# Optimization experiments

Measured on AMD Instinct MI355X. Metric: run time of the kernel, lower is better.

Reference implementation:

```python
import jax, jax.numpy as jnp
import numpy as np

B, S, D, E, TOPK = 8, 4096, 1024, 64, 2
TEMP = 0.01


def setup_inputs() -> dict:
    key = jax.random.key(0)
    k_x, k_w1, k_b1, k_w2, k_b2 = jax.random.split(key, 5)
    x = jax.random.normal(k_x, (B, S, D), dtype=jnp.float32)
    # torch.nn.Linear default init ~ U(-1/sqrt(fan_in), 1/sqrt(fan_in)); scale ok for reference
    W1 = jax.random.normal(k_w1, (D, 2 * D), dtype=jnp.float32) * (1.0 / np.sqrt(D))
    b1 = jax.random.normal(k_b1, (2 * D,), dtype=jnp.float32) * 0.01
    W2 = jax.random.normal(k_w2, (2 * D, E), dtype=jnp.float32) * (1.0 / np.sqrt(2 * D))
    b2 = jax.random.normal(k_b2, (E,), dtype=jnp.float32) * 0.01
    return {"x": x, "W1": W1, "b1": b1, "W2": W2, "b2": b2}


def reference(x, W1, b1, W2, b2):
    # 2-layer MLP router: [B,S,D] -> [B,S,2D] -> [B,S,E]
    h = jax.nn.relu(jnp.einsum('bsd,df->bsf', x, W1) + b1)
    logits = jnp.einsum('bsf,fe->bse', h, W2) + b2
    # top-k over experts
    top_k_logits, indices = jax.lax.top_k(logits, TOPK)  # [B,S,K]
    # scatter top-k logits into a -inf-filled tensor: equivalent to masking,
    # since scattered values equal logits at those positions
    keep = jax.nn.one_hot(indices, E, dtype=bool).any(axis=-2)  # [B,S,E]
    sparse_logits = jnp.where(keep, logits, -jnp.inf)
    router_output = jax.nn.softmax(sparse_logits, axis=-1)
    ori_router_output = jax.nn.softmax(logits / TEMP, axis=-1)
    return (ori_router_output, router_output, indices)
```

## Files before the change

kernel.cpp:

```cpp
#include <hip/hip_runtime.h>
#include <math.h>
#include <stdint.h>

#define M_TOK 32768
#define D_IN  1024
#define F_HID 2048
#define E_EXP 64

#define O_ORI 0
#define O_RTR (M_TOK * E_EXP)
#define O_IDX (2 * M_TOK * E_EXP)

typedef _Float16 half8 __attribute__((ext_vector_type(8)));
typedef float    f32x4 __attribute__((ext_vector_type(4)));
typedef unsigned int uint32;
typedef uint32   u32x4 __attribute__((ext_vector_type(4)));

#define WS_XH  ((size_t)0)
#define WS_XL  (WS_XH  + (size_t)M_TOK * D_IN * 2)
#define WS_W1H (WS_XL  + (size_t)M_TOK * D_IN * 2)
#define WS_W1L (WS_W1H + (size_t)D_IN * F_HID * 2)
#define WS_W2H (WS_W1L + (size_t)D_IN * F_HID * 2)
#define WS_W2L (WS_W2H + (size_t)F_HID * E_EXP * 2)
#define WS_NEED (WS_W2L + (size_t)F_HID * E_EXP * 2)

__device__ __forceinline__ void split_sc(float v, float sc, unsigned short& h, unsigned short& l) {
    const _Float16 hh = (_Float16)v;
    const float hf = (float)hh;
    const _Float16 hs = (_Float16)(hf * sc);
    const _Float16 ls = (_Float16)((v - hf) * sc);
    h = __builtin_bit_cast(unsigned short, hs);
    l = __builtin_bit_cast(unsigned short, ls);
}


__global__ void split_x_k(const float* __restrict__ x,
                          unsigned short* __restrict__ xh, unsigned short* __restrict__ xl) {
    size_t i = ((size_t)blockIdx.x * 256 + threadIdx.x) * 4;
    const float4 v = *(const float4*)&x[i];
    ushort4 h, l;
    split_sc(v.x, 64.f, h.x, l.x); split_sc(v.y, 64.f, h.y, l.y);
    split_sc(v.z, 64.f, h.z, l.z); split_sc(v.w, 64.f, h.w, l.w);
    *(ushort4*)&xh[i] = h;
    *(ushort4*)&xl[i] = l;
}

__global__ void split_w1t_k(const float* __restrict__ W1,
                            unsigned short* __restrict__ wh, unsigned short* __restrict__ wl) {
    __shared__ float t[32][33];
    const int d0 = blockIdx.x * 32;
    const int f0 = blockIdx.y * 32;
    const int r  = threadIdx.x >> 3;
    const int c4 = (threadIdx.x & 7) * 4;
    const float4 v = *(const float4*)&W1[(size_t)(d0 + r) * F_HID + f0 + c4];
    t[r][c4 + 0] = v.x; t[r][c4 + 1] = v.y; t[r][c4 + 2] = v.z; t[r][c4 + 3] = v.w;
    __syncthreads();
    ushort4 h, l;
    split_sc(t[c4 + 0][r], 64.f, h.x, l.x);
    split_sc(t[c4 + 1][r], 64.f, h.y, l.y);
    split_sc(t[c4 + 2][r], 64.f, h.z, l.z);
    split_sc(t[c4 + 3][r], 64.f, h.w, l.w);
    *(ushort4*)&wh[(size_t)(f0 + r) * D_IN + d0 + c4] = h;
    *(ushort4*)&wl[(size_t)(f0 + r) * D_IN + d0 + c4] = l;
}

__global__ void split_w2f_k(const float* __restrict__ W2,
                            unsigned short* __restrict__ wh, unsigned short* __restrict__ wl) {
    const int s  = blockIdx.x;
    const int nt = threadIdx.x >> 6;
    const int l  = threadIdx.x & 63;
    const int fb = s * 32 + (l >> 4) * 8;
    const int e  = nt * 16 + (l & 15);
    unsigned short h[8], lo[8];
#pragma unroll
    for (int j = 0; j < 8; ++j)
        split_sc(W2[(size_t)(fb + j) * E_EXP + e], 16.f, h[j], lo[j]);
    const size_t base = ((size_t)(s * 4 + nt) * 64 + l) * 8;
    ((ushort4*)&wh[base])[0] = make_ushort4(h[0], h[1], h[2], h[3]);
    ((ushort4*)&wh[base])[1] = make_ushort4(h[4], h[5], h[6], h[7]);
    ((ushort4*)&wl[base])[0] = make_ushort4(lo[0], lo[1], lo[2], lo[3]);
    ((ushort4*)&wl[base])[1] = make_ushort4(lo[4], lo[5], lo[6], lo[7]);
}


__device__ __forceinline__ uint32 swz(uint32 o) { return o ^ (((o >> 7) & 7u) << 4); }

#define STAGE16(SRCP, DSTP) \
    __builtin_amdgcn_global_load_lds((const __attribute__((address_space(1))) void*)(SRCP), \
                                     (__attribute__((address_space(3))) void*)(DSTP), 16, 0, 0)


__launch_bounds__(512, 2)
__global__ void router_one(const unsigned short* __restrict__ xh, const unsigned short* __restrict__ xl,
                           const unsigned short* __restrict__ w1h, const unsigned short* __restrict__ w1l,
                           const unsigned short* __restrict__ w2fh, const unsigned short* __restrict__ w2fl,
                           const float* __restrict__ b1, const float* __restrict__ b2,
                           float* __restrict__ out)
{
    __shared__ __align__(16) unsigned char lds[131072];

    const int tid  = threadIdx.x;
    const int lane = tid & 63;
    const int w    = tid >> 6;
    const int c15  = lane & 15;
    const int g    = lane >> 4;
    const int wr   = w >> 2;
    const int wc   = w & 3;

    const size_t tok0 = (size_t)blockIdx.x * 128;

    uint32 arow, ahalf, brow[2], bhalf[2];
    {
        const uint32 sA = swz((uint32)(tid * 16));
        arow = sA >> 6; ahalf = (sA & 63u) >> 1;
#pragma unroll
        for (int j = 0; j < 2; ++j) {
            const uint32 sB = swz((uint32)(j * 8192 + w * 1024 + lane * 16));
            brow[j] = sB >> 6; bhalf[j] = (sB & 63u) >> 1;
        }
    }

    uint32 offA[4], offB[4];
#pragma unroll
    for (int m = 0; m < 4; ++m)
        offA[m] = swz((uint32)((wr * 64 + m * 16 + c15) * 64 + g * 16));
#pragma unroll
    for (int n = 0; n < 4; ++n)
        offB[n] = swz((uint32)((wc * 64 + n * 16 + c15) * 64 + g * 16));

    f32x4 acc2[4];
#pragma unroll
    for (int nt = 0; nt < 4; ++nt) acc2[nt] = (f32x4){0.f, 0.f, 0.f, 0.f};

#define STAGE_T(T, BUF, F0) do {                                                     \
    const int d0_ = (T) * 32;                                                        \
    const size_t asrc = (tok0 + arow) * D_IN + (size_t)(d0_ + (int)ahalf);           \
    STAGE16(xh + asrc, lds + (BUF) * 16384 + w * 1024);                              \
    STAGE16(xl + asrc, lds + (BUF) * 16384 + 8192 + w * 1024);                       \
    _Pragma("unroll")                                                                \
    for (int j = 0; j < 2; ++j) {                                                    \
        const size_t bsrc = ((size_t)(F0) + brow[j]) * D_IN + (size_t)(d0_ + (int)bhalf[j]); \
        STAGE16(w1h + bsrc, lds + 32768 + (BUF) * 32768 + j * 8192 + w * 1024);      \
        STAGE16(w1l + bsrc, lds + 32768 + (BUF) * 32768 + 16384 + j * 8192 + w * 1024); \
    } } while (0)

#pragma unroll 1
    for (int fc = 0; fc < F_HID; fc += 256) {
        f32x4 acc[4][4];
#pragma unroll
        for (int m = 0; m < 4; ++m)
#pragma unroll
            for (int n = 0; n < 4; ++n) acc[m][n] = (f32x4){0.f, 0.f, 0.f, 0.f};

        __syncthreads();
        STAGE_T(0, 0, fc);
        STAGE_T(1, 1, fc);

#pragma unroll 1
        for (int t = 0; t < 32; ++t) {
            if (t < 31) asm volatile("s_waitcnt vmcnt(6)" ::: "memory");
            else        asm volatile("s_waitcnt vmcnt(0)" ::: "memory");
            __builtin_amdgcn_s_barrier();
            const unsigned char* Ab = lds + (t & 1) * 16384;
            const unsigned char* Bb = lds + 32768 + (t & 1) * 32768;

            half8 b1f[4], b2f[4];
#pragma unroll
            for (int n = 0; n < 4; ++n) {
                b1f[n] = *(const half8*)(Bb + offB[n]);
                b2f[n] = *(const half8*)(Bb + 16384 + offB[n]);
            }
            half8 a1f[2], a2f[2];
#pragma unroll
            for (int m = 0; m < 2; ++m) {
                a1f[m] = *(const half8*)(Ab + offA[m]);
                a2f[m] = *(const half8*)(Ab + 8192 + offA[m]);
            }
            __builtin_amdgcn_s_setprio(1);
#pragma unroll
            for (int m = 0; m < 2; ++m)
#pragma unroll
                for (int n = 0; n < 4; ++n) {
                    acc[m][n] = __builtin_amdgcn_mfma_f32_16x16x32_f16(a1f[m], b1f[n], acc[m][n], 0, 0, 0);
                    acc[m][n] = __builtin_amdgcn_mfma_f32_16x16x32_f16(a1f[m], b2f[n], acc[m][n], 0, 0, 0);
                    acc[m][n] = __builtin_amdgcn_mfma_f32_16x16x32_f16(a2f[m], b1f[n], acc[m][n], 0, 0, 0);
                }
            __builtin_amdgcn_s_setprio(0);
#pragma unroll
            for (int m = 0; m < 2; ++m) {
                a1f[m] = *(const half8*)(Ab + offA[2 + m]);
                a2f[m] = *(const half8*)(Ab + 8192 + offA[2 + m]);
            }
            __builtin_amdgcn_s_setprio(1);
#pragma unroll
            for (int m = 0; m < 2; ++m)
#pragma unroll
                for (int n = 0; n < 4; ++n) {
                    acc[2 + m][n] = __builtin_amdgcn_mfma_f32_16x16x32_f16(a1f[m], b1f[n], acc[2 + m][n], 0, 0, 0);
                    acc[2 + m][n] = __builtin_amdgcn_mfma_f32_16x16x32_f16(a1f[m], b2f[n], acc[2 + m][n], 0, 0, 0);
                    acc[2 + m][n] = __builtin_amdgcn_mfma_f32_16x16x32_f16(a2f[m], b1f[n], acc[2 + m][n], 0, 0, 0);
                }
            __builtin_amdgcn_s_setprio(0);
            __builtin_amdgcn_s_barrier();
            if (t + 2 < 32) STAGE_T(t + 2, t & 1, fc);
        }

        {
            float bv[4];
#pragma unroll
            for (int n = 0; n < 4; ++n) bv[n] = b1[fc + wc * 64 + n * 16 + c15];
#pragma unroll
            for (int m = 0; m < 4; ++m)
#pragma unroll
                for (int n = 0; n < 4; ++n)
#pragma unroll
                    for (int r = 0; r < 4; ++r) {
                        float hv = acc[m][n][r] * (1.f / 4096.f) + bv[n];
                        hv = fmaxf(hv, 0.f);
                        const _Float16 hh = (_Float16)hv;
                        const float hf = (float)hh;
                        const _Float16 hsv = (_Float16)(hf * 16.f);
                        const _Float16 lsv = (_Float16)((hv - hf) * 16.f);
                        const uint32 pk = (uint32)__builtin_bit_cast(unsigned short, hsv)
                                        | ((uint32)__builtin_bit_cast(unsigned short, lsv) << 16);
                        const int tok = wr * 64 + m * 16 + g * 4 + r;
                        const int fl  = wc * 64 + n * 16 + c15;
                        *(uint32*)(lds + tok * 1024 + ((fl * 4) ^ ((tok & 15) << 4))) = pk;
                    }
        }
        __syncthreads();

        {
            const int tokA = w * 16 + c15;
#pragma unroll
            for (int s = 0; s < 8; ++s) {
                const int kf = s * 32 + g * 8;
                const int sg = (fc >> 5) + s;
                half8 bf1[4], bf2[4];
#pragma unroll
                for (int nt = 0; nt < 4; ++nt) {
                    const size_t base = ((size_t)(sg * 4 + nt) * 64 + lane) * 8;
                    bf1[nt] = *(const half8*)&w2fh[base];
                    bf2[nt] = *(const half8*)&w2fl[base];
                }
                const u32x4 q0 = *(const u32x4*)(lds + tokA * 1024 + (((kf    ) * 4) ^ (c15 << 4)));
                const u32x4 q1 = *(const u32x4*)(lds + tokA * 1024 + (((kf + 4) * 4) ^ (c15 << 4)));
                u32x4 hi4, lo4;
                hi4[0] = __builtin_amdgcn_perm(q0[1], q0[0], 0x05040100u);
                hi4[1] = __builtin_amdgcn_perm(q0[3], q0[2], 0x05040100u);
                hi4[2] = __builtin_amdgcn_perm(q1[1], q1[0], 0x05040100u);
                hi4[3] = __builtin_amdgcn_perm(q1[3], q1[2], 0x05040100u);
                lo4[0] = __builtin_amdgcn_perm(q0[1], q0[0], 0x07060302u);
                lo4[1] = __builtin_amdgcn_perm(q0[3], q0[2], 0x07060302u);
                lo4[2] = __builtin_amdgcn_perm(q1[1], q1[0], 0x07060302u);
                lo4[3] = __builtin_amdgcn_perm(q1[3], q1[2], 0x07060302u);
                const half8 a1 = __builtin_bit_cast(half8, hi4);
                const half8 a2 = __builtin_bit_cast(half8, lo4);
#pragma unroll
                for (int nt = 0; nt < 4; ++nt) {
                    acc2[nt] = __builtin_amdgcn_mfma_f32_16x16x32_f16(a1, bf1[nt], acc2[nt], 0, 0, 0);
                    acc2[nt] = __builtin_amdgcn_mfma_f32_16x16x32_f16(a1, bf2[nt], acc2[nt], 0, 0, 0);
                    acc2[nt] = __builtin_amdgcn_mfma_f32_16x16x32_f16(a2, bf1[nt], acc2[nt], 0, 0, 0);
                }
            }
        }
    }
#undef STAGE_T

    __syncthreads();
    float* ls = (float*)lds;
#pragma unroll
    for (int nt = 0; nt < 4; ++nt)
#pragma unroll
        for (int r = 0; r < 4; ++r) {
            const int tl = w * 16 + g * 4 + r;
            ls[tl * 68 + nt * 16 + c15] = acc2[nt][r] * (1.f / 256.f);
        }
    __syncthreads();

    const int e = lane;
    const float be = b2[e];
#pragma unroll 1
    for (int i = 0; i < 16; ++i) {
        const float l = ls[(w * 16 + i) * 68 + e] + be;

        float v = l; int idx = e;
#pragma unroll
        for (int m = 32; m >= 1; m >>= 1) {
            const float ov = __shfl_xor(v, m, 64);
            const int   oi = __shfl_xor(idx, m, 64);
            if (ov > v || (ov == v && oi < idx)) { v = ov; idx = oi; }
        }
        const float m1 = v; const int i1 = idx;

        v = (e == i1) ? -INFINITY : l; idx = e;
#pragma unroll
        for (int m = 32; m >= 1; m >>= 1) {
            const float ov = __shfl_xor(v, m, 64);
            const int   oi = __shfl_xor(idx, m, 64);
            if (ov > v || (ov == v && oi < idx)) { v = ov; idx = oi; }
        }
        const int i2 = idx;

        const float ex = expf((l - m1) * 100.0f);
        float s = ex;
#pragma unroll
        for (int m = 32; m >= 1; m >>= 1) s += __shfl_xor(s, m, 64);
        const float ori = ex / s;

        const float q = (e == i1 || e == i2) ? expf(l - m1) : 0.f;
        float s2 = q;
#pragma unroll
        for (int m = 32; m >= 1; m >>= 1) s2 += __shfl_xor(s2, m, 64);
        const float rtr = q / s2;

        const size_t tok = tok0 + (size_t)w * 16 + i;
        out[O_ORI + tok * E_EXP + e] = ori;
        out[O_RTR + tok * E_EXP + e] = rtr;
        if (e == 0) {
            out[O_IDX + tok * 2 + 0] = (float)i1;
            out[O_IDX + tok * 2 + 1] = (float)i2;
        }
    }
}


#define BT  64
#define NB  256

__launch_bounds__(256, 2)
__global__ void router_mfma(const unsigned short* __restrict__ xh, const unsigned short* __restrict__ xl,
                            const unsigned short* __restrict__ w1h, const unsigned short* __restrict__ w1l,
                            const unsigned short* __restrict__ w2fh, const unsigned short* __restrict__ w2fl,
                            const float* __restrict__ b1, const float* __restrict__ b2,
                            float* __restrict__ out)
{
    __shared__ __align__(16) unsigned char xs_h[BT * 64];
    __shared__ __align__(16) unsigned char xs_l[BT * 64];
    __shared__ __align__(16) unsigned char w1s_h[NB * 64];
    __shared__ __align__(16) unsigned char w1s_l[NB * 64];
    __shared__ __align__(16) unsigned char hsbuf[BT * 132 * 4];

    const int tid  = threadIdx.x;
    const int lane = tid & 63;
    const int w    = tid >> 6;
    const int c15  = lane & 15;
    const int g    = lane >> 4;
    const size_t tok0 = (size_t)blockIdx.x * BT;

    uint32* hs = (uint32*)hsbuf;
    float*  ls = (float*)hsbuf;

    f32x4 acc2h[4], acc2x[4];
#pragma unroll
    for (int nt = 0; nt < 4; ++nt) {
        acc2h[nt] = (f32x4){0.f, 0.f, 0.f, 0.f};
        acc2x[nt] = (f32x4){0.f, 0.f, 0.f, 0.f};
    }

    const uint32 kqb = (uint32)g * 16u;

    for (int fc = 0; fc < F_HID; fc += NB) {
        f32x4 ahh[4][4], axx[4][4];
#pragma unroll
        for (int mt = 0; mt < 4; ++mt)
#pragma unroll
            for (int nt = 0; nt < 4; ++nt) {
                ahh[mt][nt] = (f32x4){0.f, 0.f, 0.f, 0.f};
                axx[mt][nt] = (f32x4){0.f, 0.f, 0.f, 0.f};
            }

        for (int d0 = 0; d0 < D_IN; d0 += 32) {
            __syncthreads();
            {
                uint32 o = (uint32)w * 1024u + (uint32)lane * 16u;
                uint32 s = swz(o);
                uint32 r = s >> 6, hb = (s & 63u) >> 1;
                const unsigned short* sp;
                sp = xh + (tok0 + r) * D_IN + (size_t)(d0 + (int)hb);
                STAGE16(sp, xs_h + (size_t)w * 1024);
                sp = xl + (tok0 + r) * D_IN + (size_t)(d0 + (int)hb);
                STAGE16(sp, xs_l + (size_t)w * 1024);
#pragma unroll
                for (int q = 0; q < 4; ++q) {
                    const uint32 c_ = (uint32)(q * 4 + w);
                    uint32 o2 = c_ * 1024u + (uint32)lane * 16u;
                    uint32 s2 = swz(o2);
                    uint32 r2 = s2 >> 6, hb2 = (s2 & 63u) >> 1;
                    sp = w1h + ((size_t)(fc + (int)r2)) * D_IN + (size_t)(d0 + (int)hb2);
                    STAGE16(sp, w1s_h + (size_t)c_ * 1024);
                    sp = w1l + ((size_t)(fc + (int)r2)) * D_IN + (size_t)(d0 + (int)hb2);
                    STAGE16(sp, w1s_l + (size_t)c_ * 1024);
                }
            }
            __syncthreads();

            half8 ah[4], al[4], bh[4], bl[4];
#pragma unroll
            for (int mt = 0; mt < 4; ++mt) {
                const uint32 off = swz((uint32)(mt * 16 + c15) * 64u + kqb);
                ah[mt] = *(const half8*)(xs_h + off);
                al[mt] = *(const half8*)(xs_l + off);
            }
#pragma unroll
            for (int nt = 0; nt < 4; ++nt) {
                const uint32 row = (uint32)(w * 64 + nt * 16 + c15);
                const uint32 off = swz(row * 64u + kqb);
                bh[nt] = *(const half8*)(w1s_h + off);
                bl[nt] = *(const half8*)(w1s_l + off);
            }
#pragma unroll
            for (int mt = 0; mt < 4; ++mt)
#pragma unroll
                for (int nt = 0; nt < 4; ++nt) {
                    ahh[mt][nt] = __builtin_amdgcn_mfma_f32_16x16x32_f16(ah[mt], bh[nt], ahh[mt][nt], 0, 0, 0);
                    axx[mt][nt] = __builtin_amdgcn_mfma_f32_16x16x32_f16(ah[mt], bl[nt], axx[mt][nt], 0, 0, 0);
                    axx[mt][nt] = __builtin_amdgcn_mfma_f32_16x16x32_f16(al[mt], bh[nt], axx[mt][nt], 0, 0, 0);
                }
        }

        const int fl0 = (w & 1) * 64;
#pragma unroll
        for (int phase = 0; phase < 2; ++phase) {
            if ((w >> 1) == phase) {
#pragma unroll
                for (int nt = 0; nt < 4; ++nt) {
                    const float b1v = b1[fc + w * 64 + nt * 16 + c15];
#pragma unroll
                    for (int mt = 0; mt < 4; ++mt) {
#pragma unroll
                        for (int r = 0; r < 4; ++r) {
                            float hv = (ahh[mt][nt][r] + axx[mt][nt][r]) * (1.f / 4096.f) + b1v;
                            hv = fmaxf(hv, 0.f);
                            const _Float16 hhv0 = (_Float16)hv;
                            const float hf = (float)hhv0;
                            const _Float16 hhv = (_Float16)(hf * 16.f);
                            const _Float16 hlv = (_Float16)((hv - hf) * 16.f);
                            uint32 pk = (uint32)__builtin_bit_cast(unsigned short, hhv)
                                      | ((uint32)__builtin_bit_cast(unsigned short, hlv) << 16);
                            const int t = mt * 16 + g * 4 + r;
                            hs[t * 132 + fl0 + nt * 16 + c15] = pk;
                        }
                    }
                }
            }
            __syncthreads();
            const int tA = w * 16 + c15;
#pragma unroll
            for (int ktl = 0; ktl < 4; ++ktl) {
                const u32x4 q0 = *(const u32x4*)&hs[tA * 132 + ktl * 32 + g * 8];
                const u32x4 q1 = *(const u32x4*)&hs[tA * 132 + ktl * 32 + g * 8 + 4];
                u32x4 hi4, lo4;
                hi4[0] = __builtin_amdgcn_perm(q0[1], q0[0], 0x05040100u);
                hi4[1] = __builtin_amdgcn_perm(q0[3], q0[2], 0x05040100u);
                hi4[2] = __builtin_amdgcn_perm(q1[1], q1[0], 0x05040100u);
                hi4[3] = __builtin_amdgcn_perm(q1[3], q1[2], 0x05040100u);
                lo4[0] = __builtin_amdgcn_perm(q0[1], q0[0], 0x07060302u);
                lo4[1] = __builtin_amdgcn_perm(q0[3], q0[2], 0x07060302u);
                lo4[2] = __builtin_amdgcn_perm(q1[1], q1[0], 0x07060302u);
                lo4[3] = __builtin_amdgcn_perm(q1[3], q1[2], 0x07060302u);
                const half8 a_h = __builtin_bit_cast(half8, hi4);
                const half8 a_l = __builtin_bit_cast(half8, lo4);
                const int sg = (fc >> 5) + phase * 4 + ktl;
#pragma unroll
                for (int nt = 0; nt < 4; ++nt) {
                    const size_t base = ((size_t)(sg * 4 + nt) * 64 + lane) * 8;
                    const half8 b_h = *(const half8*)&w2fh[base];
                    const half8 b_l = *(const half8*)&w2fl[base];
                    acc2h[nt] = __builtin_amdgcn_mfma_f32_16x16x32_f16(a_h, b_h, acc2h[nt], 0, 0, 0);
                    acc2x[nt] = __builtin_amdgcn_mfma_f32_16x16x32_f16(a_h, b_l, acc2x[nt], 0, 0, 0);
                    acc2x[nt] = __builtin_amdgcn_mfma_f32_16x16x32_f16(a_l, b_h, acc2x[nt], 0, 0, 0);
                }
            }
            __syncthreads();
        }
    }

#pragma unroll
    for (int nt = 0; nt < 4; ++nt)
#pragma unroll
        for (int r = 0; r < 4; ++r) {
            const int t = w * 16 + g * 4 + r;
            ls[t * 68 + nt * 16 + c15] = (acc2h[nt][r] + acc2x[nt][r]) * (1.f / 256.f);
        }
    __syncthreads();

    const int e = lane;
    const float be = b2[e];
#pragma unroll 1
    for (int i = 0; i < 16; ++i) {
        const float l = ls[(w * 16 + i) * 68 + e] + be;

        float v = l; int idx = e;
#pragma unroll
        for (int m = 32; m >= 1; m >>= 1) {
            const float ov = __shfl_xor(v, m, 64);
            const int   oi = __shfl_xor(idx, m, 64);
            if (ov > v || (ov == v && oi < idx)) { v = ov; idx = oi; }
        }
        const float m1 = v; const int i1 = idx;

        v = (e == i1) ? -INFINITY : l; idx = e;
#pragma unroll
        for (int m = 32; m >= 1; m >>= 1) {
            const float ov = __shfl_xor(v, m, 64);
            const int   oi = __shfl_xor(idx, m, 64);
            if (ov > v || (ov == v && oi < idx)) { v = ov; idx = oi; }
        }
        const int i2 = idx;

        const float ex = expf((l - m1) * 100.0f);
        float s = ex;
#pragma unroll
        for (int m = 32; m >= 1; m >>= 1) s += __shfl_xor(s, m, 64);
        const float ori = ex / s;

        const float q = (e == i1 || e == i2) ? expf(l - m1) : 0.f;
        float s2 = q;
#pragma unroll
        for (int m = 32; m >= 1; m >>= 1) s2 += __shfl_xor(s2, m, 64);
        const float rtr = q / s2;

        const size_t tok = tok0 + (size_t)w * 16 + i;
        out[O_ORI + tok * E_EXP + e] = ori;
        out[O_RTR + tok * E_EXP + e] = rtr;
        if (e == 0) {
            out[O_IDX + tok * 2 + 0] = (float)i1;
            out[O_IDX + tok * 2 + 1] = (float)i2;
        }
    }
}


extern "C" void kernel_launch(void* const* d_in, const int* in_sizes, int n_in,
                              void* d_out, int out_size, void* d_ws, size_t ws_size,
                              hipStream_t stream) {
    const float* x  = (const float*)d_in[0];
    const float* W1 = (const float*)d_in[1];
    const float* b1 = (const float*)d_in[2];
    const float* W2 = (const float*)d_in[3];
    const float* b2 = (const float*)d_in[4];
    float* out = (float*)d_out;

    unsigned char* ws = (unsigned char*)d_ws;
    unsigned short* xh  = (unsigned short*)(ws + WS_XH);
    unsigned short* xl  = (unsigned short*)(ws + WS_XL);
    unsigned short* w1h = (unsigned short*)(ws + WS_W1H);
    unsigned short* w1l = (unsigned short*)(ws + WS_W1L);
    unsigned short* w2h = (unsigned short*)(ws + WS_W2H);
    unsigned short* w2l = (unsigned short*)(ws + WS_W2L);

    hipLaunchKernelGGL(split_x_k,  dim3(M_TOK * D_IN / 4 / 256), dim3(256), 0, stream, x, xh, xl);
    hipLaunchKernelGGL(split_w1t_k, dim3(D_IN / 32, F_HID / 32), dim3(256), 0, stream, W1, w1h, w1l);
    hipLaunchKernelGGL(split_w2f_k, dim3(F_HID / 32), dim3(256), 0, stream, W2, w2h, w2l);

    if (ws_size >= WS_NEED) {
        hipLaunchKernelGGL(router_one, dim3(M_TOK / 128), dim3(512), 0, stream,
                           xh, xl, w1h, w1l, w2h, w2l, b1, b2, out);
    } else {
        hipLaunchKernelGGL(router_mfma, dim3(M_TOK / BT), dim3(256), 0, stream,
                           xh, xl, w1h, w1l, w2h, w2l, b1, b2, out);
    }
}
```

Measured before the change: 504.9 us.

## Triple-buffer W1 GEMM LDS staging and interleave loads with MFMA phases

Grows the LDS ring from two to three buffers so the next-next tile can be staged into a free buffer while the current one is read. The main loop is split into four MFMA phases, one per B column tile, with the A-tile and B-tile global→LDS copies spread between them. This aims to hide global-load issue and the LDS read latency behind matrix math instead of staging after a trailing barrier. In exchange it adds many more s_barriers and lgkmcnt waits per iteration and holds all four A fragments in registers, which raises register pressure.

```diff
diff --git a/kernel.cpp b/kernel.cpp
--- a/kernel.cpp
+++ b/kernel.cpp
@@ -90,6 +90,9 @@
                                      (__attribute__((address_space(3))) void*)(DSTP), 16, 0, 0)
 
 
+#define A_BUF(b)  ((b) * 16384)
+#define B_BUF(b)  (49152 + (b) * 32768)
+
 __launch_bounds__(512, 2)
 __global__ void router_one(const unsigned short* __restrict__ xh, const unsigned short* __restrict__ xl,
                            const unsigned short* __restrict__ w1h, const unsigned short* __restrict__ w1l,
@@ -97,7 +100,7 @@
                            const float* __restrict__ b1, const float* __restrict__ b2,
                            float* __restrict__ out)
 {
-    __shared__ __align__(16) unsigned char lds[131072];
+    __shared__ __align__(16) unsigned char lds[147456];
 
     const int tid  = threadIdx.x;
     const int lane = tid & 63;
@@ -132,17 +135,18 @@
 #pragma unroll
     for (int nt = 0; nt < 4; ++nt) acc2[nt] = (f32x4){0.f, 0.f, 0.f, 0.f};
 
-#define STAGE_T(T, BUF, F0) do {                                                     \
+#define STAGE_A(T, WB, F0) do {                                                      \
     const int d0_ = (T) * 32;                                                        \
     const size_t asrc = (tok0 + arow) * D_IN + (size_t)(d0_ + (int)ahalf);           \
-    STAGE16(xh + asrc, lds + (BUF) * 16384 + w * 1024);                              \
-    STAGE16(xl + asrc, lds + (BUF) * 16384 + 8192 + w * 1024);                       \
-    _Pragma("unroll")                                                                \
-    for (int j = 0; j < 2; ++j) {                                                    \
-        const size_t bsrc = ((size_t)(F0) + brow[j]) * D_IN + (size_t)(d0_ + (int)bhalf[j]); \
-        STAGE16(w1h + bsrc, lds + 32768 + (BUF) * 32768 + j * 8192 + w * 1024);      \
-        STAGE16(w1l + bsrc, lds + 32768 + (BUF) * 32768 + 16384 + j * 8192 + w * 1024); \
-    } } while (0)
+    STAGE16(xh + asrc, lds + A_BUF(WB) + w * 1024);                                  \
+    STAGE16(xl + asrc, lds + A_BUF(WB) + 8192 + w * 1024);                           \
+} while (0)
+#define STAGE_B(T, WB, F0, J) do {                                                   \
+    const int d0_ = (T) * 32;                                                        \
+    const size_t bsrc = ((size_t)(F0) + brow[J]) * D_IN + (size_t)(d0_ + (int)bhalf[J]); \
+    STAGE16(w1h + bsrc, lds + B_BUF(WB) + (J) * 8192 + w * 1024);                    \
+    STAGE16(w1l + bsrc, lds + B_BUF(WB) + 16384 + (J) * 8192 + w * 1024);            \
+} while (0)
 
 #pragma unroll 1
     for (int fc = 0; fc < F_HID; fc += 256) {
@@ -153,58 +157,87 @@
             for (int n = 0; n < 4; ++n) acc[m][n] = (f32x4){0.f, 0.f, 0.f, 0.f};
 
         __syncthreads();
-        STAGE_T(0, 0, fc);
-        STAGE_T(1, 1, fc);
+        STAGE_A(0, 0, fc); STAGE_B(0, 0, fc, 0); STAGE_B(0, 0, fc, 1);
+        STAGE_A(1, 1, fc); STAGE_B(1, 1, fc, 0); STAGE_B(1, 1, fc, 1);
 
 #pragma unroll 1
         for (int t = 0; t < 32; ++t) {
             if (t < 31) asm volatile("s_waitcnt vmcnt(6)" ::: "memory");
             else        asm volatile("s_waitcnt vmcnt(0)" ::: "memory");
             __builtin_amdgcn_s_barrier();
-            const unsigned char* Ab = lds + (t & 1) * 16384;
-            const unsigned char* Bb = lds + 32768 + (t & 1) * 32768;
-
-            half8 b1f[4], b2f[4];
-#pragma unroll
-            for (int n = 0; n < 4; ++n) {
-                b1f[n] = *(const half8*)(Bb + offB[n]);
-                b2f[n] = *(const half8*)(Bb + 16384 + offB[n]);
-            }
-            half8 a1f[2], a2f[2];
-#pragma unroll
-            for (int m = 0; m < 2; ++m) {
+            const int rb = t % 3;
+            const int wb = (t + 2) % 3;
+            const bool do_stage = (t + 2 < 32);
+            const unsigned char* Ab = lds + A_BUF(rb);
+            const unsigned char* Bb = lds + B_BUF(rb);
+
+            half8 a1f[4], a2f[4], b1f[4], b2f[4];
+
+#pragma unroll
+            for (int m = 0; m < 4; ++m) {
                 a1f[m] = *(const half8*)(Ab + offA[m]);
                 a2f[m] = *(const half8*)(Ab + 8192 + offA[m]);
             }
+            b1f[0] = *(const half8*)(Bb + offB[0]);
+            b2f[0] = *(const half8*)(Bb + 16384 + offB[0]);
+            if (do_stage) STAGE_A(t + 2, wb, fc);
+            __builtin_amdgcn_s_barrier();
+            asm volatile("s_waitcnt lgkmcnt(0)" ::: "memory");
             __builtin_amdgcn_s_setprio(1);
 #pragma unroll
-            for (int m = 0; m < 2; ++m)
-#pragma unroll
-                for (int n = 0; n < 4; ++n) {
-                    acc[m][n] = __builtin_amdgcn_mfma_f32_16x16x32_f16(a1f[m], b1f[n], acc[m][n], 0, 0, 0);
-                    acc[m][n] = __builtin_amdgcn_mfma_f32_16x16x32_f16(a1f[m], b2f[n], acc[m][n], 0, 0, 0);
-                    acc[m][n] = __builtin_amdgcn_mfma_f32_16x16x32_f16(a2f[m], b1f[n], acc[m][n], 0, 0, 0);
-                }
+            for (int m = 0; m < 4; ++m) {
+                acc[m][0] = __builtin_amdgcn_mfma_f32_16x16x32_f16(a1f[m], b1f[0], acc[m][0], 0, 0, 0);
+                acc[m][0] = __builtin_amdgcn_mfma_f32_16x16x32_f16(a1f[m], b2f[0], acc[m][0], 0, 0, 0);
+                acc[m][0] = __builtin_amdgcn_mfma_f32_16x16x32_f16(a2f[m], b1f[0], acc[m][0], 0, 0, 0);
+            }
             __builtin_amdgcn_s_setprio(0);
-#pragma unroll
-            for (int m = 0; m < 2; ++m) {
-                a1f[m] = *(const half8*)(Ab + offA[2 + m]);
-                a2f[m] = *(const half8*)(Ab + 8192 + offA[2 + m]);
-            }
+            __builtin_amdgcn_s_barrier();
+
+            b1f[1] = *(const half8*)(Bb + offB[1]);
+            b2f[1] = *(const half8*)(Bb + 16384 + offB[1]);
+            if (do_stage) STAGE_B(t + 2, wb, fc, 0);
+            __builtin_amdgcn_s_barrier();
+            asm volatile("s_waitcnt lgkmcnt(0)" ::: "memory");
             __builtin_amdgcn_s_setprio(1);
 #pragma unroll
-            for (int m = 0; m < 2; ++m)
-#pragma unroll
-                for (int n = 0; n < 4; ++n) {
-                    acc[2 + m][n] = __builtin_amdgcn_mfma_f32_16x16x32_f16(a1f[m], b1f[n], acc[2 + m][n], 0, 0, 0);
-                    acc[2 + m][n] = __builtin_amdgcn_mfma_f32_16x16x32_f16(a1f[m], b2f[n], acc[2 + m][n], 0, 0, 0);
-                    acc[2 + m][n] = __builtin_amdgcn_mfma_f32_16x16x32_f16(a2f[m], b1f[n], acc[2 + m][n], 0, 0, 0);
-                }
+            for (int m = 0; m < 4; ++m) {
+                acc[m][1] = __builtin_amdgcn_mfma_f32_16x16x32_f16(a1f[m], b1f[1], acc[m][1], 0, 0, 0);
+                acc[m][1] = __builtin_amdgcn_mfma_f32_16x16x32_f16(a1f[m], b2f[1], acc[m][1], 0, 0, 0);
+                acc[m][1] = __builtin_amdgcn_mfma_f32_16x16x32_f16(a2f[m], b1f[1], acc[m][1], 0, 0, 0);
+            }
             __builtin_amdgcn_s_setprio(0);
             __builtin_amdgcn_s_barrier();
-            if (t + 2 < 32) STAGE_T(t + 2, t & 1, fc);
-        }
-
+
+            b1f[2] = *(const half8*)(Bb + offB[2]);
+            b2f[2] = *(const half8*)(Bb + 16384 + offB[2]);
+            if (do_stage) STAGE_B(t + 2, wb, fc, 1);
+            __builtin_amdgcn_s_barrier();
+            asm volatile("s_waitcnt lgkmcnt(0)" ::: "memory");
+            __builtin_amdgcn_s_setprio(1);
+#pragma unroll
+            for (int m = 0; m < 4; ++m) {
+                acc[m][2] = __builtin_amdgcn_mfma_f32_16x16x32_f16(a1f[m], b1f[2], acc[m][2], 0, 0, 0);
+                acc[m][2] = __builtin_amdgcn_mfma_f32_16x16x32_f16(a1f[m], b2f[2], acc[m][2], 0, 0, 0);
+                acc[m][2] = __builtin_amdgcn_mfma_f32_16x16x32_f16(a2f[m], b1f[2], acc[m][2], 0, 0, 0);
+            }
+            __builtin_amdgcn_s_setprio(0);
+            __builtin_amdgcn_s_barrier();
+
+            b1f[3] = *(const half8*)(Bb + offB[3]);
+            b2f[3] = *(const half8*)(Bb + 16384 + offB[3]);
+            __builtin_amdgcn_s_barrier();
+            asm volatile("s_waitcnt lgkmcnt(0)" ::: "memory");
+            __builtin_amdgcn_s_setprio(1);
+#pragma unroll
+            for (int m = 0; m < 4; ++m) {
+                acc[m][3] = __builtin_amdgcn_mfma_f32_16x16x32_f16(a1f[m], b1f[3], acc[m][3], 0, 0, 0);
+                acc[m][3] = __builtin_amdgcn_mfma_f32_16x16x32_f16(a1f[m], b2f[3], acc[m][3], 0, 0, 0);
+                acc[m][3] = __builtin_amdgcn_mfma_f32_16x16x32_f16(a2f[m], b1f[3], acc[m][3], 0, 0, 0);
+            }
+            __builtin_amdgcn_s_setprio(0);
+        }
+
+        __syncthreads();
         {
             float bv[4];
 #pragma unroll
@@ -265,7 +298,8 @@
             }
         }
     }
-#undef STAGE_T
+#undef STAGE_A
+#undef STAGE_B
 
     __syncthreads();
     float* ls = (float*)lds;
```

Result: no change. 498.8 us (-1.2%).
